# Kernel optimization log

Hardware: AMD Instinct MI355X
Metric: run time of the kernel (lower is better)

The kernel has to match this reference:

```python
import jax, jax.numpy as jnp
import numpy as np

EPS = 1e-12


def _l2norm(v):
    return v / (jnp.linalg.norm(v) + EPS)


def _sn(W, u):
    """One-step power-iteration spectral normalization (torch spectral_norm, 1x1 conv weight).
    W: (out, in), u: (out,). u/v are treated as buffers (no grad)."""
    Wm = W.reshape(W.shape[0], -1)
    v = _l2norm(Wm.T @ u)
    u2 = _l2norm(Wm @ v)
    u2 = jax.lax.stop_gradient(u2)
    v = jax.lax.stop_gradient(v)
    sigma = u2 @ (Wm @ v)
    return W / sigma


def _maxpool2(x):
    # 2x2 max pool, stride 2, NCHW
    N, C, H, W = x.shape
    return x.reshape(N, C, H // 2, 2, W // 2, 2).max(axis=(3, 5))


def setup_inputs() -> dict:
    key = jax.random.key(0)
    ks = jax.random.split(key, 10)
    N, C, H, W = 16, 256, 64, 64
    s = 0.05  # keep logits moderate
    return {
        "x": jax.random.normal(ks[0], (N, C, H, W), dtype=jnp.float32),
        "Wt": jax.random.normal(ks[1], (C >> 3, C), dtype=jnp.float32) * s,
        "Wp": jax.random.normal(ks[2], (C >> 3, C), dtype=jnp.float32) * s,
        "Wg": jax.random.normal(ks[3], (C >> 1, C), dtype=jnp.float32) * s,
        "Wo": jax.random.normal(ks[4], (C, C >> 1), dtype=jnp.float32) * s,
        "ut": jax.random.normal(ks[5], (C >> 3,), dtype=jnp.float32),
        "up": jax.random.normal(ks[6], (C >> 3,), dtype=jnp.float32),
        "ug": jax.random.normal(ks[7], (C >> 1,), dtype=jnp.float32),
        "uo": jax.random.normal(ks[8], (C,), dtype=jnp.float32),
        "gamma": jnp.float32(0.1),  # nonzero so attention branch is exercised
    }


def reference(x, Wt, Wp, Wg, Wo, ut, up, ug, uo, gamma):
    N, C, H, W = x.shape
    L = H * W          # location_num
    Ld = L // 4        # downsampled_num
    # 1x1 convs as channel einsums with spectrally-normalized weights
    theta = jnp.einsum('oc,nchw->nohw', _sn(Wt, ut), x).reshape(N, C >> 3, L)
    phi = _maxpool2(jnp.einsum('oc,nchw->nohw', _sn(Wp, up), x)).reshape(N, C >> 3, Ld)
    attn = jax.nn.softmax(jnp.einsum('ncl,ncm->nlm', theta, phi), axis=-1)  # (N, L, Ld)
    g = _maxpool2(jnp.einsum('oc,nchw->nohw', _sn(Wg, ug), x)).reshape(N, C >> 1, Ld)
    attn_g = jnp.einsum('ncm,nlm->ncl', g, attn).reshape(N, C >> 1, H, W)
    attn_g = jnp.einsum('oc,nchw->nohw', _sn(Wo, uo), attn_g)
    return x + gamma * attn_g
```

## Files before the change

### kernel.cpp

```cpp
#include <hip/hip_runtime.h>
#include <math.h>

#define EPS 1e-12f

typedef unsigned short ushort_t;
typedef __attribute__((ext_vector_type(8))) short short8;
typedef __attribute__((ext_vector_type(4))) float f32x4;
typedef __attribute__((ext_vector_type(4))) unsigned short ushort4v;
typedef __attribute__((ext_vector_type(2))) unsigned int uint2v;

#define WS_WB_F 0
#define WS_WO_F 24576
#define WS_TH_F 40960
#define WS_PH_F 1089536
#define WS_G_F  1351680

__device__ __forceinline__ ushort_t f2bf(float f) {
  unsigned int u = __float_as_uint(f);
  u += 0x7fffu + ((u >> 16) & 1u);
  return (ushort_t)(u >> 16);
}
__device__ __forceinline__ float bf2f(ushort_t u) {
  return __uint_as_float(((unsigned int)u) << 16);
}
__device__ __forceinline__ unsigned int pack_bf2(float lo, float hi) {
  return (unsigned int)f2bf(lo) | ((unsigned int)f2bf(hi) << 16);
}

__device__ __forceinline__ void gload_lds16(const ushort_t* g, ushort_t* l) {
  __builtin_amdgcn_global_load_lds(
      (const __attribute__((address_space(1))) unsigned int*)g,
      (__attribute__((address_space(3))) unsigned int*)l, 16, 0, 0);
}

__device__ __forceinline__ float block_reduce_sum(float v, float* red) {
  int t = threadIdx.x;
  red[t] = v;
  __syncthreads();
  #pragma unroll
  for (int s = 128; s > 0; s >>= 1) {
    if (t < s) red[t] += red[t + s];
    __syncthreads();
  }
  float r = red[0];
  __syncthreads();
  return r;
}

__global__ __launch_bounds__(256) void sn_kernel(
    const float* __restrict__ Wt, const float* __restrict__ Wp,
    const float* __restrict__ Wg, const float* __restrict__ Wo,
    const float* __restrict__ ut, const float* __restrict__ up,
    const float* __restrict__ ug, const float* __restrict__ uo,
    float* __restrict__ ws) {
  __shared__ float red[256];
  __shared__ float ub[256];
  __shared__ float vb[256];
  const float* W; const float* u; int O, Ci;
  switch (blockIdx.x) {
    case 0:  W = Wt; u = ut; O = 32;  Ci = 256; break;
    case 1:  W = Wp; u = up; O = 32;  Ci = 256; break;
    case 2:  W = Wg; u = ug; O = 128; Ci = 256; break;
    default: W = Wo; u = uo; O = 256; Ci = 128; break;
  }
  int t = threadIdx.x;
  if (t < O) ub[t] = u[t];
  __syncthreads();
  float tv = 0.f;
  if (t < Ci) {
    for (int o = 0; o < O; o++) tv += W[o * Ci + t] * ub[o];
  }
  float nt2 = block_reduce_sum((t < Ci) ? tv * tv : 0.f, red);
  float ntn = sqrtf(nt2);
  if (t < Ci) vb[t] = tv / (ntn + EPS);
  __syncthreads();
  float sv = 0.f;
  if (t < O) {
    const float* Wr = W + (size_t)t * Ci;
    for (int c = 0; c < Ci; c += 4) {
      float4 wv = *(const float4*)(Wr + c);
      sv += wv.x * vb[c] + wv.y * vb[c + 1] + wv.z * vb[c + 2] + wv.w * vb[c + 3];
    }
  }
  float ss = block_reduce_sum((t < O) ? sv * sv : 0.f, red);
  float ns = sqrtf(ss);
  float sigma = ss / (ns + EPS);
  float inv = 1.f / sigma;
  int total = O * Ci;
  if (blockIdx.x == 3) {
    ushort_t* dst = (ushort_t*)(ws + WS_WO_F);
    for (int i = t; i < total; i += 256) {
      int o = i >> 7, c = i & 127;
      int oct = o >> 4, l16o = o & 15, kc = c >> 5, qd = (c >> 3) & 3, j = c & 7;
      dst[(((kc * 16 + oct) * 64 + qd * 16 + l16o) << 3) + j] = f2bf(W[i] * inv);
    }
  } else {
    int base_row = (blockIdx.x == 0) ? 0 : (blockIdx.x == 1 ? 32 : 64);
    ushort_t* dst = (ushort_t*)(ws + WS_WB_F);
    for (int i = t; i < total; i += 256) {
      int o = i >> 8, c = i & 255;
      int og = base_row + o;
      int mtg = og >> 4, l16o = og & 15, kc = c >> 5, qd = (c >> 3) & 3, j = c & 7;
      dst[(((mtg * 8 + kc) * 64 + qd * 16 + l16o) << 3) + j] = f2bf(W[i] * inv);
    }
  }
}

__global__ __launch_bounds__(256, 2) void proj_mfma(
    const float* __restrict__ x, const ushort_t* __restrict__ wb,
    ushort_t* __restrict__ theta_b, ushort_t* __restrict__ phi_b,
    ushort_t* __restrict__ g_b) {
  __shared__ ushort_t xb[128 * 264];
  const int t = threadIdx.x;
  const int n = blockIdx.y;
  const int l0 = blockIdx.x * 128;
  const float* xn = x + ((size_t)n * 256) * 4096 + l0;
  {
    const int lrel = t & 127;
    const int half = t >> 7;
    #pragma unroll 4
    for (int ch = 0; ch < 16; ++ch) {
      int chunk = half * 16 + ch;
      short8 v;
      #pragma unroll
      for (int j = 0; j < 8; ++j) {
        float f = xn[(size_t)(chunk * 8 + j) * 4096 + lrel];
        v[j] = (short)f2bf(f);
      }
      *(short8*)(&xb[lrel * 264 + chunk * 8]) = v;
    }
  }
  __syncthreads();
  const int w = t >> 6;
  const int lane = t & 63;
  const int quad = lane >> 4;
  const int l16 = lane & 15;
  const int rowA = (w * 16 + l16) * 264;
  const int rowB = (64 + w * 16 + l16) * 264;
  const int hd = blockIdx.x;
  #pragma unroll 1
  for (int pass = 0; pass < 2; ++pass) {
    f32x4 accA[6], accB[6];
    #pragma unroll
    for (int i = 0; i < 6; ++i) {
      accA[i] = (f32x4){0.f, 0.f, 0.f, 0.f};
      accB[i] = (f32x4){0.f, 0.f, 0.f, 0.f};
    }
    #pragma unroll
    for (int kc = 0; kc < 8; ++kc) {
      short8 bA = *(const short8*)(&xb[rowA + kc * 32 + quad * 8]);
      short8 bB = *(const short8*)(&xb[rowB + kc * 32 + quad * 8]);
      #pragma unroll
      for (int mt = 0; mt < 6; ++mt) {
        int mtg = pass * 6 + mt;
        short8 aW = *(const short8*)(wb + (((size_t)(mtg * 8 + kc) * 64 + lane) << 3));
        accA[mt] = __builtin_amdgcn_mfma_f32_16x16x32_bf16(aW, bA, accA[mt], 0, 0, 0);
        accB[mt] = __builtin_amdgcn_mfma_f32_16x16x32_bf16(aW, bB, accB[mt], 0, 0, 0);
      }
    }
    #pragma unroll
    for (int mt = 0; mt < 6; ++mt) {
      int mtg = pass * 6 + mt;
      if (mtg < 2) {
        int lA = l0 + w * 16 + l16;
        ushort4v vA, vB;
        #pragma unroll
        for (int r = 0; r < 4; ++r) { vA[r] = f2bf(accA[mt][r]); vB[r] = f2bf(accB[mt][r]); }
        *(ushort4v*)(theta_b + ((size_t)n * 4096 + lA) * 32 + mtg * 16 + quad * 4) = vA;
        *(ushort4v*)(theta_b + ((size_t)n * 4096 + lA + 64) * 32 + mtg * 16 + quad * 4) = vB;
      } else {
        float pm[4];
        #pragma unroll
        for (int r = 0; r < 4; ++r) {
          float v = fmaxf(accA[mt][r], accB[mt][r]);
          v = fmaxf(v, __shfl_xor(v, 1));
          pm[r] = v;
        }
        if ((l16 & 1) == 0) {
          int m = hd * 32 + w * 8 + (l16 >> 1);
          if (mtg < 4) {
            ushort4v vv;
            #pragma unroll
            for (int r = 0; r < 4; ++r) vv[r] = f2bf(pm[r]);
            *(ushort4v*)(phi_b + ((size_t)n * 1024 + m) * 32 + (mtg - 2) * 16 + quad * 4) = vv;
          } else {
            int cg0 = (mtg - 4) * 16 + quad * 4;
            #pragma unroll
            for (int r = 0; r < 4; ++r)
              g_b[((size_t)n * 128 + cg0 + r) * 1024 + m] = f2bf(pm[r]);
          }
        }
      }
    }
  }
}

__global__ __launch_bounds__(256, 4) void attn_mfma(
    const float* __restrict__ x,
    const ushort_t* __restrict__ theta_b,
    const ushort_t* __restrict__ phi_b,
    const ushort_t* __restrict__ g_b,
    const ushort_t* __restrict__ Wo_fb,
    const float* __restrict__ gamma_p,
    float* __restrict__ out) {
  __shared__ __align__(16) unsigned char smem[39936];
  ushort_t* g_lds = (ushort_t*)smem;
  ushort_t* outb  = (ushort_t*)smem;

  const int t = threadIdx.x;
  const int w = t >> 6;
  const int lane = t & 63;
  const int quad = lane >> 4;
  const int l16 = lane & 15;
  unsigned int* pw = (unsigned int*)(smem + 34816) + w * 320;

  const int flat = blockIdx.y * 64 + blockIdx.x;
  const int nf = ((flat & 7) << 7) | (flat >> 3);
  const int n = nf >> 6;
  const int l0 = (nf & 63) << 6;
  const int lq = l0 + w * 16;

  const short8 b_th = *(const short8*)(theta_b + ((size_t)n * 4096 + lq + l16) * 32 + quad * 8);
  const ushort_t* phiN = phi_b + (size_t)n * 1024 * 32;
  const ushort_t* gN   = g_b + (size_t)n * 128 * 1024;

  const int row_l = lane >> 4;
  const int s_even = (lane & 15) ^ row_l;

  f32x4 oacc[8];
  #pragma unroll
  for (int j = 0; j < 8; ++j) oacc[j] = (f32x4){0.f, 0.f, 0.f, 0.f};
  float M = -3.0e38f, L = 0.f;

  #pragma unroll 1
  for (int mc = 0; mc < 8; ++mc) {
    const int m0 = mc * 128;
    __syncthreads();
    #pragma unroll
    for (int b8 = 0; b8 < 8; ++b8) {
      int blk = w * 8 + b8;
      int slot = s_even ^ ((b8 & 1) << 2);
      const ushort_t* src = gN + (size_t)(4 * blk + row_l) * 1024 + m0 + slot * 8;
      gload_lds16(src, g_lds + blk * 512);
    }
    f32x4 st[8];
    const f32x4 z = (f32x4){0.f, 0.f, 0.f, 0.f};
    #pragma unroll
    for (int i = 0; i < 8; ++i) {
      short8 aph = *(const short8*)(phiN + (size_t)(m0 + i * 16 + l16) * 32 + quad * 8);
      st[i] = __builtin_amdgcn_mfma_f32_16x16x32_bf16(aph, b_th, z, 0, 0, 0);
    }
    f32x4 m4 = st[0];
    #pragma unroll
    for (int i = 1; i < 8; ++i) {
      #pragma unroll
      for (int r = 0; r < 4; ++r) m4[r] = fmaxf(m4[r], st[i][r]);
    }
    float mx = fmaxf(fmaxf(m4[0], m4[1]), fmaxf(m4[2], m4[3]));
    mx = fmaxf(mx, __shfl_xor(mx, 16));
    mx = fmaxf(mx, __shfl_xor(mx, 32));
    float nm = fmaxf(M, mx);
    float alpha = __expf(M - nm);
    M = nm;
    #pragma unroll
    for (int i = 0; i < 8; ++i) {
      #pragma unroll
      for (int r = 0; r < 4; ++r) st[i][r] = __expf(st[i][r] - nm);
    }
    f32x4 s4 = st[0];
    #pragma unroll
    for (int i = 1; i < 8; ++i) {
      #pragma unroll
      for (int r = 0; r < 4; ++r) s4[r] += st[i][r];
    }
    float psum = (s4[0] + s4[1]) + (s4[2] + s4[3]);
    psum += __shfl_xor(psum, 16);
    psum += __shfl_xor(psum, 32);
    L = L * alpha + psum;
    #pragma unroll
    for (int j = 0; j < 8; ++j) {
      #pragma unroll
      for (int r = 0; r < 4; ++r) oacc[j][r] *= alpha;
    }
    unsigned int pk[16];
    #pragma unroll
    for (int i = 0; i < 8; ++i) {
      pk[2 * i]     = pack_bf2(st[i][0], st[i][1]);
      pk[2 * i + 1] = pack_bf2(st[i][2], st[i][3]);
    }
    __syncthreads();
    #pragma unroll
    for (int s = 0; s < 4; ++s) {
      *(uint2v*)&pw[l16 * 20 + quad * 2]     = (uint2v){pk[4 * s],     pk[4 * s + 1]};
      *(uint2v*)&pw[l16 * 20 + 8 + quad * 2] = (uint2v){pk[4 * s + 2], pk[4 * s + 3]};
      short8 pb = *(const short8*)&pw[l16 * 20 + quad * 4];
      #pragma unroll
      for (int j = 0; j < 8; ++j) {
        int row = j * 16 + l16;
        int pslot = (s * 4 + quad) ^ (l16 & 7);
        short8 gf = *(const short8*)(g_lds + row * 128 + pslot * 8);
        oacc[j] = __builtin_amdgcn_mfma_f32_16x16x32_bf16(gf, pb, oacc[j], 0, 0, 0);
      }
    }
  }
  __syncthreads();

  const float invL = 1.f / L;
  #pragma unroll 1
  for (int half = 0; half < 2; ++half) {
    f32x4 acc2[8];
    #pragma unroll
    for (int i = 0; i < 8; ++i) acc2[i] = (f32x4){0.f, 0.f, 0.f, 0.f};
    #pragma unroll
    for (int kc = 0; kc < 4; ++kc) {
      unsigned int e0 = pack_bf2(oacc[2 * kc][0] * invL, oacc[2 * kc][1] * invL);
      unsigned int e1 = pack_bf2(oacc[2 * kc][2] * invL, oacc[2 * kc][3] * invL);
      unsigned int e2 = pack_bf2(oacc[2 * kc + 1][0] * invL, oacc[2 * kc + 1][1] * invL);
      unsigned int e3 = pack_bf2(oacc[2 * kc + 1][2] * invL, oacc[2 * kc + 1][3] * invL);
      *(uint2v*)&pw[l16 * 20 + quad * 2]     = (uint2v){e0, e1};
      *(uint2v*)&pw[l16 * 20 + 8 + quad * 2] = (uint2v){e2, e3};
      short8 aO = *(const short8*)&pw[l16 * 20 + quad * 4];
      #pragma unroll
      for (int o8 = 0; o8 < 8; ++o8) {
        int oct = half * 8 + o8;
        short8 bw = *(const short8*)(Wo_fb + (((size_t)(kc * 16 + oct) * 64 + lane) << 3));
        acc2[o8] = __builtin_amdgcn_mfma_f32_16x16x32_bf16(aO, bw, acc2[o8], 0, 0, 0);
      }
    }
    #pragma unroll
    for (int o8 = 0; o8 < 8; ++o8) {
      int oct = half * 8 + o8;
      #pragma unroll
      for (int r = 0; r < 4; ++r)
        outb[(oct * 16 + l16) * 68 + w * 16 + quad * 4 + r] = f2bf(acc2[o8][r]);
    }
  }
  __syncthreads();
  {
    const float gm = gamma_p[0];
    const int oc = (t >> 4);
    const int lch = (t & 15) * 4;
    #pragma unroll
    for (int ocg = 0; ocg < 16; ++ocg) {
      int row = ocg * 16 + oc;
      ushort4v ov = *(const ushort4v*)(&outb[row * 68 + lch]);
      const float* xp = x + ((size_t)n * 256 + row) * 4096 + l0 + lch;
      float* op = out + ((size_t)n * 256 + row) * 4096 + l0 + lch;
      float4 xv = *(const float4*)xp;
      float4 v;
      v.x = xv.x + gm * bf2f(ov[0]);
      v.y = xv.y + gm * bf2f(ov[1]);
      v.z = xv.z + gm * bf2f(ov[2]);
      v.w = xv.w + gm * bf2f(ov[3]);
      *(float4*)op = v;
    }
  }
}

extern "C" void kernel_launch(void* const* d_in, const int* in_sizes, int n_in,
                              void* d_out, int out_size, void* d_ws, size_t ws_size,
                              hipStream_t stream) {
  const float* x  = (const float*)d_in[0];
  const float* Wt = (const float*)d_in[1];
  const float* Wp = (const float*)d_in[2];
  const float* Wg = (const float*)d_in[3];
  const float* Wo = (const float*)d_in[4];
  const float* ut = (const float*)d_in[5];
  const float* up = (const float*)d_in[6];
  const float* ug = (const float*)d_in[7];
  const float* uo = (const float*)d_in[8];
  const float* gamma = (const float*)d_in[9];
  float* ws  = (float*)d_ws;
  float* out = (float*)d_out;

  ushort_t* wb      = (ushort_t*)(ws + WS_WB_F);
  ushort_t* Wo_b    = (ushort_t*)(ws + WS_WO_F);
  ushort_t* theta_b = (ushort_t*)(ws + WS_TH_F);
  ushort_t* phi_b   = (ushort_t*)(ws + WS_PH_F);
  ushort_t* g_b     = (ushort_t*)(ws + WS_G_F);

  sn_kernel<<<4, 256, 0, stream>>>(Wt, Wp, Wg, Wo, ut, up, ug, uo, ws);
  proj_mfma<<<dim3(32, 16), 256, 0, stream>>>(x, wb, theta_b, phi_b, g_b);
  attn_mfma<<<dim3(64, 16), 256, 0, stream>>>(x, theta_b, phi_b, g_b, Wo_b, gamma, out);
}
```

Measured before the change: 209.2 us.

## Process two query tiles per wave and double-buffer g staging in LDS

Each wave now handles 32 query rows (two 16-row tiles) instead of 16, so each phi fragment and each g fragment read from LDS feeds two MFMAs. The grid is halved to match. The g tile for the next key chunk is staged into a second LDS buffer while the current chunk is consumed, with s_setprio raised around the MFMA loop. The LDS layout of g is simplified to match the MFMA fragment order. The costs are higher register and LDS use (launch bounds drop to 2 blocks), fewer blocks in flight, and a larger output stage.

Measured after the change: 219.9 us. +5.1%, slower.

```diff
diff --git a/kernel.cpp b/kernel.cpp
--- a/kernel.cpp
+++ b/kernel.cpp
@@ -195,7 +195,59 @@
   }
 }
 
-__global__ __launch_bounds__(256, 4) void attn_mfma(
+__device__ __forceinline__ void stage_g(const ushort_t* gN, ushort_t* buf,
+                                        int m0, int w, int l16, int quad) {
+  #pragma unroll
+  for (int b = 0; b < 8; ++b) {
+    int idx = w * 8 + b;
+    int j = idx >> 2, s = idx & 3;
+    const ushort_t* src = gN + (size_t)(j * 16 + l16) * 1024 + m0 + s * 32 + quad * 8;
+    gload_lds16(src, buf + (j * 4 + s) * 512);
+  }
+}
+
+__device__ __forceinline__ void softmax_step(f32x4* st, float& M, float& L,
+                                             f32x4* oa, unsigned int* pk) {
+  f32x4 m4 = st[0];
+  #pragma unroll
+  for (int i = 1; i < 8; ++i) {
+    #pragma unroll
+    for (int r = 0; r < 4; ++r) m4[r] = fmaxf(m4[r], st[i][r]);
+  }
+  float mx = fmaxf(fmaxf(m4[0], m4[1]), fmaxf(m4[2], m4[3]));
+  mx = fmaxf(mx, __shfl_xor(mx, 16));
+  mx = fmaxf(mx, __shfl_xor(mx, 32));
+  float nm = fmaxf(M, mx);
+  float alpha = __expf(M - nm);
+  M = nm;
+  #pragma unroll
+  for (int i = 0; i < 8; ++i) {
+    #pragma unroll
+    for (int r = 0; r < 4; ++r) st[i][r] = __expf(st[i][r] - nm);
+  }
+  f32x4 s4 = st[0];
+  #pragma unroll
+  for (int i = 1; i < 8; ++i) {
+    #pragma unroll
+    for (int r = 0; r < 4; ++r) s4[r] += st[i][r];
+  }
+  float ps = (s4[0] + s4[1]) + (s4[2] + s4[3]);
+  ps += __shfl_xor(ps, 16);
+  ps += __shfl_xor(ps, 32);
+  L = L * alpha + ps;
+  #pragma unroll
+  for (int j = 0; j < 8; ++j) {
+    #pragma unroll
+    for (int r = 0; r < 4; ++r) oa[j][r] *= alpha;
+  }
+  #pragma unroll
+  for (int i = 0; i < 8; ++i) {
+    pk[2 * i]     = pack_bf2(st[i][0], st[i][1]);
+    pk[2 * i + 1] = pack_bf2(st[i][2], st[i][3]);
+  }
+}
+
+__global__ __launch_bounds__(256, 2) void attn_mfma(
     const float* __restrict__ x,
     const ushort_t* __restrict__ theta_b,
     const ushort_t* __restrict__ phi_b,
@@ -203,8 +255,9 @@
     const ushort_t* __restrict__ Wo_fb,
     const float* __restrict__ gamma_p,
     float* __restrict__ out) {
-  __shared__ __align__(16) unsigned char smem[39936];
-  ushort_t* g_lds = (ushort_t*)smem;
+  __shared__ __align__(16) unsigned char smem[77824];
+  ushort_t* gbuf0 = (ushort_t*)smem;
+  ushort_t* gbuf1 = (ushort_t*)(smem + 32768);
   ushort_t* outb  = (ushort_t*)smem;
 
   const int t = threadIdx.x;
@@ -212,140 +265,112 @@
   const int lane = t & 63;
   const int quad = lane >> 4;
   const int l16 = lane & 15;
-  unsigned int* pw = (unsigned int*)(smem + 34816) + w * 320;
-
-  const int flat = blockIdx.y * 64 + blockIdx.x;
-  const int nf = ((flat & 7) << 7) | (flat >> 3);
-  const int n = nf >> 6;
-  const int l0 = (nf & 63) << 6;
-  const int lq = l0 + w * 16;
-
-  const short8 b_th = *(const short8*)(theta_b + ((size_t)n * 4096 + lq + l16) * 32 + quad * 8);
+  unsigned int* pw0 = (unsigned int*)(smem + 67584) + w * 640;
+  unsigned int* pw1 = pw0 + 320;
+
+  const int flat = blockIdx.y * 32 + blockIdx.x;
+  const int nf = ((flat & 7) << 6) | (flat >> 3);
+  const int n = nf >> 5;
+  const int l0 = (nf & 31) << 7;
+  const int lqw = l0 + w * 32;
+
+  const short8 bth0 = *(const short8*)(theta_b + ((size_t)n * 4096 + lqw + l16) * 32 + quad * 8);
+  const short8 bth1 = *(const short8*)(theta_b + ((size_t)n * 4096 + lqw + 16 + l16) * 32 + quad * 8);
   const ushort_t* phiN = phi_b + (size_t)n * 1024 * 32;
   const ushort_t* gN   = g_b + (size_t)n * 128 * 1024;
 
-  const int row_l = lane >> 4;
-  const int s_even = (lane & 15) ^ row_l;
-
-  f32x4 oacc[8];
-  #pragma unroll
-  for (int j = 0; j < 8; ++j) oacc[j] = (f32x4){0.f, 0.f, 0.f, 0.f};
-  float M = -3.0e38f, L = 0.f;
+  f32x4 oacc0[8], oacc1[8];
+  #pragma unroll
+  for (int j = 0; j < 8; ++j) {
+    oacc0[j] = (f32x4){0.f, 0.f, 0.f, 0.f};
+    oacc1[j] = (f32x4){0.f, 0.f, 0.f, 0.f};
+  }
+  float M0 = -3.0e38f, L0v = 0.f, M1 = -3.0e38f, L1v = 0.f;
+
+  stage_g(gN, gbuf0, 0, w, l16, quad);
 
   #pragma unroll 1
   for (int mc = 0; mc < 8; ++mc) {
     const int m0 = mc * 128;
+    ushort_t* cbuf = (mc & 1) ? gbuf1 : gbuf0;
+    ushort_t* nbuf = (mc & 1) ? gbuf0 : gbuf1;
+    short8 aph[8];
+    #pragma unroll
+    for (int i = 0; i < 8; ++i)
+      aph[i] = *(const short8*)(phiN + (size_t)(m0 + i * 16 + l16) * 32 + quad * 8);
+    const f32x4 z = (f32x4){0.f, 0.f, 0.f, 0.f};
+    f32x4 st0[8], st1[8];
+    #pragma unroll
+    for (int i = 0; i < 8; ++i) {
+      st0[i] = __builtin_amdgcn_mfma_f32_16x16x32_bf16(aph[i], bth0, z, 0, 0, 0);
+      st1[i] = __builtin_amdgcn_mfma_f32_16x16x32_bf16(aph[i], bth1, z, 0, 0, 0);
+    }
+    unsigned int pk0[16], pk1[16];
+    softmax_step(st0, M0, L0v, oacc0, pk0);
+    softmax_step(st1, M1, L1v, oacc1, pk1);
     __syncthreads();
-    #pragma unroll
-    for (int b8 = 0; b8 < 8; ++b8) {
-      int blk = w * 8 + b8;
-      int slot = s_even ^ ((b8 & 1) << 2);
-      const ushort_t* src = gN + (size_t)(4 * blk + row_l) * 1024 + m0 + slot * 8;
-      gload_lds16(src, g_lds + blk * 512);
-    }
-    f32x4 st[8];
-    const f32x4 z = (f32x4){0.f, 0.f, 0.f, 0.f};
-    #pragma unroll
-    for (int i = 0; i < 8; ++i) {
-      short8 aph = *(const short8*)(phiN + (size_t)(m0 + i * 16 + l16) * 32 + quad * 8);
-      st[i] = __builtin_amdgcn_mfma_f32_16x16x32_bf16(aph, b_th, z, 0, 0, 0);
-    }
-    f32x4 m4 = st[0];
-    #pragma unroll
-    for (int i = 1; i < 8; ++i) {
-      #pragma unroll
-      for (int r = 0; r < 4; ++r) m4[r] = fmaxf(m4[r], st[i][r]);
-    }
-    float mx = fmaxf(fmaxf(m4[0], m4[1]), fmaxf(m4[2], m4[3]));
-    mx = fmaxf(mx, __shfl_xor(mx, 16));
-    mx = fmaxf(mx, __shfl_xor(mx, 32));
-    float nm = fmaxf(M, mx);
-    float alpha = __expf(M - nm);
-    M = nm;
-    #pragma unroll
-    for (int i = 0; i < 8; ++i) {
-      #pragma unroll
-      for (int r = 0; r < 4; ++r) st[i][r] = __expf(st[i][r] - nm);
-    }
-    f32x4 s4 = st[0];
-    #pragma unroll
-    for (int i = 1; i < 8; ++i) {
-      #pragma unroll
-      for (int r = 0; r < 4; ++r) s4[r] += st[i][r];
-    }
-    float psum = (s4[0] + s4[1]) + (s4[2] + s4[3]);
-    psum += __shfl_xor(psum, 16);
-    psum += __shfl_xor(psum, 32);
-    L = L * alpha + psum;
-    #pragma unroll
-    for (int j = 0; j < 8; ++j) {
-      #pragma unroll
-      for (int r = 0; r < 4; ++r) oacc[j][r] *= alpha;
-    }
-    unsigned int pk[16];
-    #pragma unroll
-    for (int i = 0; i < 8; ++i) {
-      pk[2 * i]     = pack_bf2(st[i][0], st[i][1]);
-      pk[2 * i + 1] = pack_bf2(st[i][2], st[i][3]);
-    }
-    __syncthreads();
+    if (mc < 7) stage_g(gN, nbuf, m0 + 128, w, l16, quad);
+    __builtin_amdgcn_s_setprio(1);
     #pragma unroll
     for (int s = 0; s < 4; ++s) {
-      *(uint2v*)&pw[l16 * 20 + quad * 2]     = (uint2v){pk[4 * s],     pk[4 * s + 1]};
-      *(uint2v*)&pw[l16 * 20 + 8 + quad * 2] = (uint2v){pk[4 * s + 2], pk[4 * s + 3]};
-      short8 pb = *(const short8*)&pw[l16 * 20 + quad * 4];
+      *(uint2v*)&pw0[l16 * 20 + quad * 2]     = (uint2v){pk0[4 * s],     pk0[4 * s + 1]};
+      *(uint2v*)&pw0[l16 * 20 + 8 + quad * 2] = (uint2v){pk0[4 * s + 2], pk0[4 * s + 3]};
+      *(uint2v*)&pw1[l16 * 20 + quad * 2]     = (uint2v){pk1[4 * s],     pk1[4 * s + 1]};
+      *(uint2v*)&pw1[l16 * 20 + 8 + quad * 2] = (uint2v){pk1[4 * s + 2], pk1[4 * s + 3]};
+      short8 pb0 = *(const short8*)&pw0[l16 * 20 + quad * 4];
+      short8 pb1 = *(const short8*)&pw1[l16 * 20 + quad * 4];
       #pragma unroll
       for (int j = 0; j < 8; ++j) {
-        int row = j * 16 + l16;
-        int pslot = (s * 4 + quad) ^ (l16 & 7);
-        short8 gf = *(const short8*)(g_lds + row * 128 + pslot * 8);
-        oacc[j] = __builtin_amdgcn_mfma_f32_16x16x32_bf16(gf, pb, oacc[j], 0, 0, 0);
+        short8 gf = *(const short8*)(cbuf + (size_t)(j * 4 + s) * 512 + lane * 8);
+        oacc0[j] = __builtin_amdgcn_mfma_f32_16x16x32_bf16(gf, pb0, oacc0[j], 0, 0, 0);
+        oacc1[j] = __builtin_amdgcn_mfma_f32_16x16x32_bf16(gf, pb1, oacc1[j], 0, 0, 0);
       }
     }
-  }
-  __syncthreads();
-
-  const float invL = 1.f / L;
-  #pragma unroll 1
-  for (int half = 0; half < 2; ++half) {
-    f32x4 acc2[8];
-    #pragma unroll
-    for (int i = 0; i < 8; ++i) acc2[i] = (f32x4){0.f, 0.f, 0.f, 0.f};
+    __builtin_amdgcn_s_setprio(0);
+  }
+  __syncthreads();
+
+  #pragma unroll
+  for (int qg = 0; qg < 2; ++qg) {
+    f32x4* oa = qg ? oacc1 : oacc0;
+    unsigned int* pwq = qg ? pw1 : pw0;
+    const float invL = 1.f / (qg ? L1v : L0v);
+    f32x4 acc2[16];
+    #pragma unroll
+    for (int i = 0; i < 16; ++i) acc2[i] = (f32x4){0.f, 0.f, 0.f, 0.f};
     #pragma unroll
     for (int kc = 0; kc < 4; ++kc) {
-      unsigned int e0 = pack_bf2(oacc[2 * kc][0] * invL, oacc[2 * kc][1] * invL);
-      unsigned int e1 = pack_bf2(oacc[2 * kc][2] * invL, oacc[2 * kc][3] * invL);
-      unsigned int e2 = pack_bf2(oacc[2 * kc + 1][0] * invL, oacc[2 * kc + 1][1] * invL);
-      unsigned int e3 = pack_bf2(oacc[2 * kc + 1][2] * invL, oacc[2 * kc + 1][3] * invL);
-      *(uint2v*)&pw[l16 * 20 + quad * 2]     = (uint2v){e0, e1};
-      *(uint2v*)&pw[l16 * 20 + 8 + quad * 2] = (uint2v){e2, e3};
-      short8 aO = *(const short8*)&pw[l16 * 20 + quad * 4];
+      unsigned int e0 = pack_bf2(oa[2 * kc][0] * invL, oa[2 * kc][1] * invL);
+      unsigned int e1 = pack_bf2(oa[2 * kc][2] * invL, oa[2 * kc][3] * invL);
+      unsigned int e2 = pack_bf2(oa[2 * kc + 1][0] * invL, oa[2 * kc + 1][1] * invL);
+      unsigned int e3 = pack_bf2(oa[2 * kc + 1][2] * invL, oa[2 * kc + 1][3] * invL);
+      *(uint2v*)&pwq[l16 * 20 + quad * 2]     = (uint2v){e0, e1};
+      *(uint2v*)&pwq[l16 * 20 + 8 + quad * 2] = (uint2v){e2, e3};
+      short8 aO = *(const short8*)&pwq[l16 * 20 + quad * 4];
       #pragma unroll
-      for (int o8 = 0; o8 < 8; ++o8) {
-        int oct = half * 8 + o8;
+      for (int oct = 0; oct < 16; ++oct) {
         short8 bw = *(const short8*)(Wo_fb + (((size_t)(kc * 16 + oct) * 64 + lane) << 3));
-        acc2[o8] = __builtin_amdgcn_mfma_f32_16x16x32_bf16(aO, bw, acc2[o8], 0, 0, 0);
+        acc2[oct] = __builtin_amdgcn_mfma_f32_16x16x32_bf16(aO, bw, acc2[oct], 0, 0, 0);
       }
     }
     #pragma unroll
-    for (int o8 = 0; o8 < 8; ++o8) {
-      int oct = half * 8 + o8;
+    for (int oct = 0; oct < 16; ++oct) {
       #pragma unroll
       for (int r = 0; r < 4; ++r)
-        outb[(oct * 16 + l16) * 68 + w * 16 + quad * 4 + r] = f2bf(acc2[o8][r]);
+        outb[(oct * 16 + l16) * 132 + w * 32 + qg * 16 + quad * 4 + r] = f2bf(acc2[oct][r]);
     }
   }
   __syncthreads();
   {
     const float gm = gamma_p[0];
-    const int oc = (t >> 4);
-    const int lch = (t & 15) * 4;
-    #pragma unroll
-    for (int ocg = 0; ocg < 16; ++ocg) {
-      int row = ocg * 16 + oc;
-      ushort4v ov = *(const ushort4v*)(&outb[row * 68 + lch]);
-      const float* xp = x + ((size_t)n * 256 + row) * 4096 + l0 + lch;
-      float* op = out + ((size_t)n * 256 + row) * 4096 + l0 + lch;
+    const int lid = t & 31;
+    const int ocr = t >> 5;
+    #pragma unroll 8
+    for (int ocg = 0; ocg < 32; ++ocg) {
+      int row = ocg * 8 + ocr;
+      ushort4v ov = *(const ushort4v*)(&outb[row * 132 + lid * 4]);
+      const float* xp = x + ((size_t)n * 256 + row) * 4096 + l0 + lid * 4;
+      float* op = out + ((size_t)n * 256 + row) * 4096 + l0 + lid * 4;
       float4 xv = *(const float4*)xp;
       float4 v;
       v.x = xv.x + gm * bf2f(ov[0]);
@@ -381,5 +406,5 @@
 
   sn_kernel<<<4, 256, 0, stream>>>(Wt, Wp, Wg, Wo, ut, up, ug, uo, ws);
   proj_mfma<<<dim3(32, 16), 256, 0, stream>>>(x, wb, theta_b, phi_b, g_b);
-  attn_mfma<<<dim3(64, 16), 256, 0, stream>>>(x, theta_b, phi_b, g_b, Wo_b, gamma, out);
-}
+  attn_mfma<<<dim3(32, 16), 256, 0, stream>>>(x, theta_b, phi_b, g_b, Wo_b, gamma, out);
+}
```

## Pre-swizzle g and phi into MFMA fragment layout, drop LDS staging in attention

Applied to the files above, without the earlier changes.

The projection kernel now writes g directly in MFMA fragment order and permutes phi rows, so the attention kernel can read g fragments straight from global memory and build the P operand in registers. This removes the LDS staging, the P transpose through LDS, and the per-chunk barriers. The Wo layout is permuted to match the register-resident operand. Softmax now works in base 2: log2(e) is folded into the theta weight and a raw hardware exp2 is used. Other changes are cheaper round-half-up bf16 packing, setprio around the MFMA loop, and a single 16-wide output projection pass. The costs are more global/L2 traffic for g, since each block rereads it with no LDS reuse, more register pressure, and slightly different rounding.

New measurement: 224.6 us. +7.4%, slower.

```diff
diff --git a/kernel.cpp b/kernel.cpp
--- a/kernel.cpp
+++ b/kernel.cpp
@@ -8,6 +8,7 @@
 typedef __attribute__((ext_vector_type(4))) float f32x4;
 typedef __attribute__((ext_vector_type(4))) unsigned short ushort4v;
 typedef __attribute__((ext_vector_type(2))) unsigned int uint2v;
+typedef __attribute__((ext_vector_type(4))) unsigned int uint32x4;
 
 #define WS_WB_F 0
 #define WS_WO_F 24576
@@ -23,14 +24,15 @@
 __device__ __forceinline__ float bf2f(ushort_t u) {
   return __uint_as_float(((unsigned int)u) << 16);
 }
-__device__ __forceinline__ unsigned int pack_bf2(float lo, float hi) {
-  return (unsigned int)f2bf(lo) | ((unsigned int)f2bf(hi) << 16);
-}
-
-__device__ __forceinline__ void gload_lds16(const ushort_t* g, ushort_t* l) {
-  __builtin_amdgcn_global_load_lds(
-      (const __attribute__((address_space(1))) unsigned int*)g,
-      (__attribute__((address_space(3))) unsigned int*)l, 16, 0, 0);
+__device__ __forceinline__ unsigned int pack_bfrh(float lo, float hi) {
+  unsigned int a = __float_as_uint(lo) + 0x8000u;
+  unsigned int b = __float_as_uint(hi) + 0x8000u;
+  return (a >> 16) | (b & 0xffff0000u);
+}
+__device__ __forceinline__ float exp2_hw(float x) {
+  float r;
+  asm("v_exp_f32 %0, %1" : "=v"(r) : "v"(x));
+  return r;
 }
 
 __device__ __forceinline__ float block_reduce_sum(float v, float* red) {
@@ -86,13 +88,17 @@
   float ns = sqrtf(ss);
   float sigma = ss / (ns + EPS);
   float inv = 1.f / sigma;
+  if (blockIdx.x == 0) inv *= 1.44269504088896f;
   int total = O * Ci;
   if (blockIdx.x == 3) {
     ushort_t* dst = (ushort_t*)(ws + WS_WO_F);
     for (int i = t; i < total; i += 256) {
       int o = i >> 7, c = i & 127;
-      int oct = o >> 4, l16o = o & 15, kc = c >> 5, qd = (c >> 3) & 3, j = c & 7;
-      dst[(((kc * 16 + oct) * 64 + qd * 16 + l16o) << 3) + j] = f2bf(W[i] * inv);
+      int oct = o >> 4, l16o = o & 15, kc = c >> 5, cl = c & 31;
+      int kap = (cl < 16) ? ((cl >> 2) * 8 + (cl & 3))
+                          : (((cl >> 2) & 3) * 8 + 4 + (cl & 3));
+      dst[(((kc * 16 + oct) * 64 + (kap >> 3) * 16 + l16o) << 3) + (kap & 7)] =
+          f2bf(W[i] * inv);
     }
   } else {
     int base_row = (blockIdx.x == 0) ? 0 : (blockIdx.x == 1 ? 32 : 64);
@@ -109,7 +115,7 @@
 __global__ __launch_bounds__(256, 2) void proj_mfma(
     const float* __restrict__ x, const ushort_t* __restrict__ wb,
     ushort_t* __restrict__ theta_b, ushort_t* __restrict__ phi_b,
-    ushort_t* __restrict__ g_b) {
+    ushort_t* __restrict__ g_fb) {
   __shared__ ushort_t xb[128 * 264];
   const int t = threadIdx.x;
   const int n = blockIdx.y;
@@ -177,17 +183,19 @@
           pm[r] = v;
         }
         if ((l16 & 1) == 0) {
-          int m = hd * 32 + w * 8 + (l16 >> 1);
+          int rr = l16 >> 1;
           if (mtg < 4) {
+            int mp = hd * 32 + ((rr & 4) ? 16 : 0) + w * 4 + (rr & 3);
             ushort4v vv;
             #pragma unroll
             for (int r = 0; r < 4; ++r) vv[r] = f2bf(pm[r]);
-            *(ushort4v*)(phi_b + ((size_t)n * 1024 + m) * 32 + (mtg - 2) * 16 + quad * 4) = vv;
+            *(ushort4v*)(phi_b + ((size_t)n * 1024 + mp) * 32 + (mtg - 2) * 16 + quad * 4) = vv;
           } else {
-            int cg0 = (mtg - 4) * 16 + quad * 4;
+            size_t fb = (size_t)n * 131072 +
+                        (size_t)((hd * 8 + (mtg - 4)) * 64 + w * 16 + quad * 4) * 8 + rr;
             #pragma unroll
             for (int r = 0; r < 4; ++r)
-              g_b[((size_t)n * 128 + cg0 + r) * 1024 + m] = f2bf(pm[r]);
+              g_fb[fb + (size_t)r * 8] = f2bf(pm[r]);
           }
         }
       }
@@ -199,20 +207,17 @@
     const float* __restrict__ x,
     const ushort_t* __restrict__ theta_b,
     const ushort_t* __restrict__ phi_b,
-    const ushort_t* __restrict__ g_b,
+    const ushort_t* __restrict__ g_fb,
     const ushort_t* __restrict__ Wo_fb,
     const float* __restrict__ gamma_p,
     float* __restrict__ out) {
-  __shared__ __align__(16) unsigned char smem[39936];
-  ushort_t* g_lds = (ushort_t*)smem;
-  ushort_t* outb  = (ushort_t*)smem;
+  __shared__ ushort_t outb[256 * 68];
 
   const int t = threadIdx.x;
   const int w = t >> 6;
   const int lane = t & 63;
   const int quad = lane >> 4;
   const int l16 = lane & 15;
-  unsigned int* pw = (unsigned int*)(smem + 34816) + w * 320;
 
   const int flat = blockIdx.y * 64 + blockIdx.x;
   const int nf = ((flat & 7) << 7) | (flat >> 3);
@@ -220,12 +225,9 @@
   const int l0 = (nf & 63) << 6;
   const int lq = l0 + w * 16;
 
-  const short8 b_th = *(const short8*)(theta_b + ((size_t)n * 4096 + lq + l16) * 32 + quad * 8);
+  const short8 bth = *(const short8*)(theta_b + ((size_t)n * 4096 + lq + l16) * 32 + quad * 8);
   const ushort_t* phiN = phi_b + (size_t)n * 1024 * 32;
-  const ushort_t* gN   = g_b + (size_t)n * 128 * 1024;
-
-  const int row_l = lane >> 4;
-  const int s_even = (lane & 15) ^ row_l;
+  const ushort_t* gN   = g_fb + (size_t)n * 131072;
 
   f32x4 oacc[8];
   #pragma unroll
@@ -235,48 +237,41 @@
   #pragma unroll 1
   for (int mc = 0; mc < 8; ++mc) {
     const int m0 = mc * 128;
-    __syncthreads();
-    #pragma unroll
-    for (int b8 = 0; b8 < 8; ++b8) {
-      int blk = w * 8 + b8;
-      int slot = s_even ^ ((b8 & 1) << 2);
-      const ushort_t* src = gN + (size_t)(4 * blk + row_l) * 1024 + m0 + slot * 8;
-      gload_lds16(src, g_lds + blk * 512);
-    }
+    const f32x4 z = (f32x4){0.f, 0.f, 0.f, 0.f};
     f32x4 st[8];
-    const f32x4 z = (f32x4){0.f, 0.f, 0.f, 0.f};
     #pragma unroll
     for (int i = 0; i < 8; ++i) {
       short8 aph = *(const short8*)(phiN + (size_t)(m0 + i * 16 + l16) * 32 + quad * 8);
-      st[i] = __builtin_amdgcn_mfma_f32_16x16x32_bf16(aph, b_th, z, 0, 0, 0);
-    }
-    f32x4 m4 = st[0];
-    #pragma unroll
-    for (int i = 1; i < 8; ++i) {
-      #pragma unroll
-      for (int r = 0; r < 4; ++r) m4[r] = fmaxf(m4[r], st[i][r]);
-    }
-    float mx = fmaxf(fmaxf(m4[0], m4[1]), fmaxf(m4[2], m4[3]));
+      st[i] = __builtin_amdgcn_mfma_f32_16x16x32_bf16(aph, bth, z, 0, 0, 0);
+    }
+    f32x4 a0 = st[0], a1 = st[1], a2 = st[2], a3 = st[3];
+    #pragma unroll
+    for (int r = 0; r < 4; ++r) {
+      a0[r] = fmaxf(a0[r], st[4][r]); a1[r] = fmaxf(a1[r], st[5][r]);
+      a2[r] = fmaxf(a2[r], st[6][r]); a3[r] = fmaxf(a3[r], st[7][r]);
+    }
+    #pragma unroll
+    for (int r = 0; r < 4; ++r) { a0[r] = fmaxf(a0[r], a2[r]); a1[r] = fmaxf(a1[r], a3[r]); }
+    float mx = fmaxf(fmaxf(fmaxf(a0[0], a1[0]), fmaxf(a0[1], a1[1])),
+                     fmaxf(fmaxf(a0[2], a1[2]), fmaxf(a0[3], a1[3])));
     mx = fmaxf(mx, __shfl_xor(mx, 16));
     mx = fmaxf(mx, __shfl_xor(mx, 32));
     float nm = fmaxf(M, mx);
-    float alpha = __expf(M - nm);
+    float alpha = exp2_hw(M - nm);
     M = nm;
     #pragma unroll
     for (int i = 0; i < 8; ++i) {
       #pragma unroll
-      for (int r = 0; r < 4; ++r) st[i][r] = __expf(st[i][r] - nm);
-    }
-    f32x4 s4 = st[0];
-    #pragma unroll
-    for (int i = 1; i < 8; ++i) {
-      #pragma unroll
-      for (int r = 0; r < 4; ++r) s4[r] += st[i][r];
-    }
-    float psum = (s4[0] + s4[1]) + (s4[2] + s4[3]);
-    psum += __shfl_xor(psum, 16);
-    psum += __shfl_xor(psum, 32);
-    L = L * alpha + psum;
+      for (int r = 0; r < 4; ++r) st[i][r] = exp2_hw(st[i][r] - nm);
+    }
+    f32x4 s0 = st[0], s1 = st[1];
+    #pragma unroll
+    for (int r = 0; r < 4; ++r) {
+      s0[r] += st[2][r] + st[4][r] + st[6][r];
+      s1[r] += st[3][r] + st[5][r] + st[7][r];
+    }
+    float ps = (s0[0] + s1[0]) + (s0[1] + s1[1]) + (s0[2] + s1[2]) + (s0[3] + s1[3]);
+    L = L * alpha + ps;
     #pragma unroll
     for (int j = 0; j < 8; ++j) {
       #pragma unroll
@@ -285,55 +280,49 @@
     unsigned int pk[16];
     #pragma unroll
     for (int i = 0; i < 8; ++i) {
-      pk[2 * i]     = pack_bf2(st[i][0], st[i][1]);
-      pk[2 * i + 1] = pack_bf2(st[i][2], st[i][3]);
-    }
-    __syncthreads();
+      pk[2 * i]     = pack_bfrh(st[i][0], st[i][1]);
+      pk[2 * i + 1] = pack_bfrh(st[i][2], st[i][3]);
+    }
+    __builtin_amdgcn_s_setprio(1);
     #pragma unroll
     for (int s = 0; s < 4; ++s) {
-      *(uint2v*)&pw[l16 * 20 + quad * 2]     = (uint2v){pk[4 * s],     pk[4 * s + 1]};
-      *(uint2v*)&pw[l16 * 20 + 8 + quad * 2] = (uint2v){pk[4 * s + 2], pk[4 * s + 3]};
-      short8 pb = *(const short8*)&pw[l16 * 20 + quad * 4];
+      uint32x4 u = {pk[4 * s], pk[4 * s + 1], pk[4 * s + 2], pk[4 * s + 3]};
+      short8 pb = __builtin_bit_cast(short8, u);
       #pragma unroll
       for (int j = 0; j < 8; ++j) {
-        int row = j * 16 + l16;
-        int pslot = (s * 4 + quad) ^ (l16 & 7);
-        short8 gf = *(const short8*)(g_lds + row * 128 + pslot * 8);
+        short8 gf = *(const short8*)(gN + (((size_t)((mc * 4 + s) * 8 + j) * 64 + lane) << 3));
         oacc[j] = __builtin_amdgcn_mfma_f32_16x16x32_bf16(gf, pb, oacc[j], 0, 0, 0);
       }
     }
-  }
-  __syncthreads();
-
+    __builtin_amdgcn_s_setprio(0);
+  }
+
+  L += __shfl_xor(L, 16);
+  L += __shfl_xor(L, 32);
   const float invL = 1.f / L;
-  #pragma unroll 1
-  for (int half = 0; half < 2; ++half) {
-    f32x4 acc2[8];
-    #pragma unroll
-    for (int i = 0; i < 8; ++i) acc2[i] = (f32x4){0.f, 0.f, 0.f, 0.f};
-    #pragma unroll
-    for (int kc = 0; kc < 4; ++kc) {
-      unsigned int e0 = pack_bf2(oacc[2 * kc][0] * invL, oacc[2 * kc][1] * invL);
-      unsigned int e1 = pack_bf2(oacc[2 * kc][2] * invL, oacc[2 * kc][3] * invL);
-      unsigned int e2 = pack_bf2(oacc[2 * kc + 1][0] * invL, oacc[2 * kc + 1][1] * invL);
-      unsigned int e3 = pack_bf2(oacc[2 * kc + 1][2] * invL, oacc[2 * kc + 1][3] * invL);
-      *(uint2v*)&pw[l16 * 20 + quad * 2]     = (uint2v){e0, e1};
-      *(uint2v*)&pw[l16 * 20 + 8 + quad * 2] = (uint2v){e2, e3};
-      short8 aO = *(const short8*)&pw[l16 * 20 + quad * 4];
-      #pragma unroll
-      for (int o8 = 0; o8 < 8; ++o8) {
-        int oct = half * 8 + o8;
-        short8 bw = *(const short8*)(Wo_fb + (((size_t)(kc * 16 + oct) * 64 + lane) << 3));
-        acc2[o8] = __builtin_amdgcn_mfma_f32_16x16x32_bf16(aO, bw, acc2[o8], 0, 0, 0);
-      }
-    }
-    #pragma unroll
-    for (int o8 = 0; o8 < 8; ++o8) {
-      int oct = half * 8 + o8;
-      #pragma unroll
-      for (int r = 0; r < 4; ++r)
-        outb[(oct * 16 + l16) * 68 + w * 16 + quad * 4 + r] = f2bf(acc2[o8][r]);
-    }
+  f32x4 acc2[16];
+  #pragma unroll
+  for (int i = 0; i < 16; ++i) acc2[i] = (f32x4){0.f, 0.f, 0.f, 0.f};
+  #pragma unroll
+  for (int kc = 0; kc < 4; ++kc) {
+    uint32x4 u;
+    u[0] = pack_bfrh(oacc[2 * kc][0] * invL, oacc[2 * kc][1] * invL);
+    u[1] = pack_bfrh(oacc[2 * kc][2] * invL, oacc[2 * kc][3] * invL);
+    u[2] = pack_bfrh(oacc[2 * kc + 1][0] * invL, oacc[2 * kc + 1][1] * invL);
+    u[3] = pack_bfrh(oacc[2 * kc + 1][2] * invL, oacc[2 * kc + 1][3] * invL);
+    short8 aO = __builtin_bit_cast(short8, u);
+    #pragma unroll
+    for (int oct = 0; oct < 16; ++oct) {
+      short8 bw = *(const short8*)(Wo_fb + (((size_t)(kc * 16 + oct) * 64 + lane) << 3));
+      acc2[oct] = __builtin_amdgcn_mfma_f32_16x16x32_bf16(aO, bw, acc2[oct], 0, 0, 0);
+    }
+  }
+  #pragma unroll
+  for (int oct = 0; oct < 16; ++oct) {
+    uint2v p2;
+    p2[0] = pack_bfrh(acc2[oct][0], acc2[oct][1]);
+    p2[1] = pack_bfrh(acc2[oct][2], acc2[oct][3]);
+    *(uint2v*)(&outb[(oct * 16 + l16) * 68 + w * 16 + quad * 4]) = p2;
   }
   __syncthreads();
   {
@@ -377,9 +366,9 @@
   ushort_t* Wo_b    = (ushort_t*)(ws + WS_WO_F);
   ushort_t* theta_b = (ushort_t*)(ws + WS_TH_F);
   ushort_t* phi_b   = (ushort_t*)(ws + WS_PH_F);
-  ushort_t* g_b     = (ushort_t*)(ws + WS_G_F);
+  ushort_t* g_fb    = (ushort_t*)(ws + WS_G_F);
 
   sn_kernel<<<4, 256, 0, stream>>>(Wt, Wp, Wg, Wo, ut, up, ug, uo, ws);
-  proj_mfma<<<dim3(32, 16), 256, 0, stream>>>(x, wb, theta_b, phi_b, g_b);
-  attn_mfma<<<dim3(64, 16), 256, 0, stream>>>(x, theta_b, phi_b, g_b, Wo_b, gamma, out);
-}
+  proj_mfma<<<dim3(32, 16), 256, 0, stream>>>(x, wb, theta_b, phi_b, g_fb);
+  attn_mfma<<<dim3(64, 16), 256, 0, stream>>>(x, theta_b, phi_b, g_fb, Wo_b, gamma, out);
+}
```
